# Performance work log

Hardware: AMD Instinct MI355X
Metric: run time of the kernel (lower is better)

The kernel has to match this reference:

```python
import jax, jax.numpy as jnp
import numpy as np

V = 6890   # SMPL vertices
J = 24     # SMPL joints
NB = 10    # betas
P = 207    # pose blendshape basis = (J-1)*9
B = 1024
PARENTS = np.array([-1, 0, 0, 0, 1, 2, 3, 4, 5, 6, 7, 8, 9, 9, 9, 12, 13, 14, 16, 17, 18, 19, 20, 21])


def setup_inputs() -> dict:
    key = jax.random.key(0)
    ks = jax.random.split(key, 9)
    pose_axis_angle = jax.random.normal(ks[0], (B, 69), dtype=jnp.float32) * 0.2
    betas = jax.random.normal(ks[1], (B, NB), dtype=jnp.float32)
    global_orient = jax.random.normal(ks[2], (B, 3), dtype=jnp.float32) * 0.2
    v_template = jax.random.normal(ks[3], (V, 3), dtype=jnp.float32)
    shapedirs = jax.random.normal(ks[4], (V, 3, NB), dtype=jnp.float32) * 0.01
    posedirs = jax.random.normal(ks[5], (P, V * 3), dtype=jnp.float32) * 0.01
    jr = jax.random.uniform(ks[6], (J, V), dtype=jnp.float32)
    J_regressor = jr / jr.sum(-1, keepdims=True)
    jr17 = jax.random.uniform(ks[7], (17, V), dtype=jnp.float32)
    J_regressor_h36m = jr17 / jr17.sum(-1, keepdims=True)
    w = jax.random.uniform(ks[8], (V, J), dtype=jnp.float32)
    lbs_weights = w / w.sum(-1, keepdims=True)
    return {
        'pose_axis_angle': pose_axis_angle, 'betas': betas, 'global_orient': global_orient,
        'v_template': v_template, 'shapedirs': shapedirs, 'posedirs': posedirs,
        'J_regressor': J_regressor, 'J_regressor_h36m': J_regressor_h36m,
        'lbs_weights': lbs_weights,
    }


def rodrigues(rvec):
    # rvec: [N,3] axis-angle -> [N,3,3] rotation matrices
    angle = jnp.linalg.norm(rvec + 1e-8, axis=-1, keepdims=True)  # [N,1]
    axis = rvec / angle
    s = jnp.sin(angle)[..., None]
    c = jnp.cos(angle)[..., None]
    rx, ry, rz = axis[..., 0], axis[..., 1], axis[..., 2]
    z = jnp.zeros_like(rx)
    K = jnp.stack([z, -rz, ry, rz, z, -rx, -ry, rx, z], axis=-1).reshape(-1, 3, 3)
    I = jnp.eye(3, dtype=rvec.dtype)
    return I + s * K + (1.0 - c) * (K @ K)


def _lbs(pose_axis_angle, betas, global_orient, v_template, shapedirs, posedirs,
         J_regressor, J_regressor_h36m, lbs_weights):
    b = betas.shape[0]
    full_pose = jnp.concatenate([global_orient, pose_axis_angle], axis=1)  # [B,72]
    # shape blendshapes
    v_shaped = v_template + jnp.einsum('bl,vkl->bvk', betas, shapedirs)    # [B,V,3]
    Jrest = jnp.einsum('jv,bvk->bjk', J_regressor, v_shaped)               # [B,J,3]
    # pose to rotation matrices
    rot_mats = rodrigues(full_pose.reshape(-1, 3)).reshape(b, J, 3, 3)
    I3 = jnp.eye(3, dtype=rot_mats.dtype)
    pose_feature = (rot_mats[:, 1:] - I3).reshape(b, P)                    # [B,207]
    v_posed = v_shaped + (pose_feature @ posedirs).reshape(b, V, 3)
    # kinematic tree FK
    rel = Jrest.at[:, 1:].add(-Jrest[:, PARENTS[1:]])                      # relative joint offsets
    T = (jnp.zeros((b, J, 4, 4), dtype=rot_mats.dtype)
         .at[..., :3, :3].set(rot_mats)
         .at[..., :3, 3].set(rel)
         .at[..., 3, 3].set(1.0))
    chain = [T[:, 0]]
    for i in range(1, J):
        chain.append(chain[int(PARENTS[i])] @ T[:, i])
    G = jnp.stack(chain, axis=1)                                           # [B,J,4,4]
    posed_joints = G[:, :, :3, 3]
    # remove rest-pose joint locations to get skinning transforms
    A = G.at[:, :, :3, 3].add(-jnp.einsum('bjmn,bjn->bjm', G[:, :, :3, :3], Jrest))
    # linear blend skinning
    Tv = jnp.einsum('vj,bjmn->bvmn', lbs_weights, A)                       # [B,V,4,4]
    verts = jnp.einsum('bvmn,bvn->bvm', Tv[:, :, :3, :3], v_posed) + Tv[:, :, :3, 3]
    joints_from_verts = jnp.einsum('jv,bvk->bjk', J_regressor_h36m, verts)
    return verts, posed_joints, rot_mats, joints_from_verts


def reference(pose_axis_angle, betas, global_orient, v_template, shapedirs, posedirs,
              J_regressor, J_regressor_h36m, lbs_weights):
    verts, joints, rot_mats, jfv = _lbs(pose_axis_angle, betas, global_orient, v_template,
                                        shapedirs, posedirs, J_regressor, J_regressor_h36m,
                                        lbs_weights)
    # transl is None -> root-center (root is detached in torch)
    root = jax.lax.stop_gradient(joints[:, :1])
    root17 = jax.lax.stop_gradient(jfv[:, :1])
    return verts - root, joints - root, rot_mats, jfv - root17
```

## Files before the change

kernel.cpp:

```cpp
#include <hip/hip_runtime.h>
#include <hip/hip_bf16.h>

constexpr int kB  = 1024;
constexpr int kV  = 6890;
constexpr int kJ  = 24;
constexpr int kNB = 10;
constexpr int kP  = 207;
constexpr int kH  = 17;

constexpr int kN   = kV * 3;
constexpr int kKP  = 224;
constexpr int kNT  = 1296;
constexpr int kNP  = kNT * 16;
constexpr int kVC  = 862;
constexpr int kTB  = 4;

constexpr int kJsBlocks = kJ * 8;
constexpr int kPbBlocks = kNP / 64;
constexpr int kVB = (kV + 255) / 256;
constexpr int kJB  = 4;

constexpr size_t O_VERTS  = 0;
constexpr size_t O_JOINTS = (size_t)kB * kV * 3;
constexpr size_t O_ROT    = O_JOINTS + (size_t)kB * kJ * 3;
constexpr size_t O_JFV    = O_ROT + (size_t)kB * kJ * 9;

constexpr size_t WS_JSP  = 0;
constexpr size_t WS_A    = 8192;
constexpr size_t WS_ROOT = WS_A + (size_t)kB * 288;
constexpr size_t WS_ASWZ = WS_ROOT + 4096;
constexpr size_t WS_BSWZ = WS_ASWZ + 114688;

typedef __attribute__((ext_vector_type(8))) short short8;
typedef __attribute__((ext_vector_type(4))) float float4v;

__device__ __forceinline__ unsigned short f2bf(float f) {
    unsigned u = __float_as_uint(f);
    unsigned r = (u + 0x7FFFu + ((u >> 16) & 1u)) >> 16;
    return (unsigned short)r;
}

__device__ __forceinline__ bool amb0_is_weights(const float* __restrict__ amb0) {
    float s = 0.f;
    #pragma unroll
    for (int i = 0; i < kJ; i++) s += amb0[i];
    return fabsf(s - 1.0f) < 0.5f;
}

__device__ __forceinline__ size_t a_idx(int mtile, int minr, int k) {
    int kt = k >> 5, quad = (k >> 3) & 3, kin = k & 7;
    return ((size_t)(mtile * 7 + kt)) * 512 + (size_t)(quad * 128 + minr * 8 + kin);
}

__global__ __launch_bounds__(256) void k_sfb(
    const float* __restrict__ amb0,
    const float* __restrict__ amb1,
    const float* __restrict__ sd,
    const float* __restrict__ vt,
    const float* __restrict__ pd,
    float* __restrict__ partial,
    unsigned short* __restrict__ bswz)
{
    __shared__ unsigned short lds[kKP][68];
    __shared__ float red[4][33];

    int t = threadIdx.x;

    if (blockIdx.x < kJsBlocks) {
        const float* Jreg = amb0_is_weights(amb0) ? amb1 : amb0;
        int j = blockIdx.x >> 3;
        int c = blockIdx.x & 7;
        int lane = t & 63;
        int wave = t >> 6;

        float acc[33];
        #pragma unroll
        for (int i = 0; i < 33; i++) acc[i] = 0.f;

        int vend = min(kVC * (c + 1), kV);
        for (int v = kVC * c + t; v < vend; v += 256) {
            float w = Jreg[j * kV + v];
            const float* sdp = sd + (size_t)v * 30;
            #pragma unroll
            for (int k = 0; k < 3; k++) {
                #pragma unroll
                for (int l = 0; l < kNB; l++)
                    acc[k * 11 + l] += w * sdp[k * 10 + l];
                acc[k * 11 + 10] += w * vt[v * 3 + k];
            }
        }
        #pragma unroll
        for (int off = 32; off > 0; off >>= 1) {
            #pragma unroll
            for (int i = 0; i < 33; i++)
                acc[i] += __shfl_down(acc[i], off, 64);
        }
        if (lane == 0) {
            #pragma unroll
            for (int i = 0; i < 33; i++) red[wave][i] = acc[i];
        }
        __syncthreads();
        if (t < 33) {
            float s = red[0][t] + red[1][t] + red[2][t] + red[3][t];
            partial[((size_t)j * 8 + c) * 33 + t] = s;
        }
    } else {
        int g = blockIdx.x - kJsBlocks;
        int n0 = g * 64;

        for (int kbase = 0; kbase < kKP; kbase += 4) {
            int k = kbase + (t >> 6);
            int nl = t & 63;
            int n = n0 + nl;
            float val = 0.f;
            if (n < kN) {
                if (k < kP)                 val = pd[(size_t)k * kN + n];
                else if (k < kP + kNB)      val = sd[(size_t)n * kNB + (k - kP)];
                else if (k == kP + kNB)     val = vt[n];
            }
            lds[k][nl] = f2bf(val);
        }
        __syncthreads();

        #pragma unroll 1
        for (int tt = 0; tt < 4; tt++) {
            int ntile = g * 4 + tt;
            #pragma unroll 1
            for (int kt = 0; kt < 7; kt++) {
                size_t base = ((size_t)ntile * 7 + kt) * 512;
                #pragma unroll
                for (int u = 0; u < 2; u++) {
                    int e = t * 2 + u;
                    int quad = e >> 7, rem = e & 127;
                    int nin = rem >> 3, kin = rem & 7;
                    int k = kt * 32 + quad * 8 + kin;
                    bswz[base + e] = lds[k][tt * 16 + nin];
                }
            }
        }
    }
}

__global__ __launch_bounds__(64) void k_pose(
    const float* __restrict__ pose,
    const float* __restrict__ betas,
    const float* __restrict__ gor,
    const float* __restrict__ jsp,
    float* __restrict__ wsA,
    float* __restrict__ wsRoot,
    unsigned short* __restrict__ aswz,
    float* __restrict__ out)
{
    __shared__ float Rsh[kJ][9];
    __shared__ float Jr[kJ][3];
    __shared__ float G[kJ][12];

    int b = blockIdx.x;
    int t = threadIdx.x;
    int mtile = b >> 4, minr = b & 15;

    if (t < kJ) {
        float rx, ry, rz;
        if (t == 0) {
            rx = gor[b * 3 + 0]; ry = gor[b * 3 + 1]; rz = gor[b * 3 + 2];
        } else {
            int o = b * 69 + (t - 1) * 3;
            rx = pose[o]; ry = pose[o + 1]; rz = pose[o + 2];
        }
        float ex = rx + 1e-8f, ey = ry + 1e-8f, ez = rz + 1e-8f;
        float ang = sqrtf(ex * ex + ey * ey + ez * ez);
        float x = rx / ang, y = ry / ang, z = rz / ang;
        float s = sinf(ang), c = cosf(ang), oc = 1.0f - c;
        float r[9];
        r[0] = 1.0f - oc * (y * y + z * z);
        r[1] = -s * z + oc * (x * y);
        r[2] =  s * y + oc * (x * z);
        r[3] =  s * z + oc * (x * y);
        r[4] = 1.0f - oc * (x * x + z * z);
        r[5] = -s * x + oc * (y * z);
        r[6] = -s * y + oc * (x * z);
        r[7] =  s * x + oc * (y * z);
        r[8] = 1.0f - oc * (x * x + y * y);
        #pragma unroll
        for (int i = 0; i < 9; i++) Rsh[t][i] = r[i];
        float* ro = out + O_ROT + (size_t)b * (kJ * 9) + (size_t)t * 9;
        #pragma unroll
        for (int i = 0; i < 9; i++) ro[i] = r[i];
        if (t >= 1) {
            #pragma unroll
            for (int i = 0; i < 9; i++) {
                int k = (t - 1) * 9 + i;
                float val = r[i] - ((i == 0 || i == 4 || i == 8) ? 1.0f : 0.0f);
                aswz[a_idx(mtile, minr, k)] = f2bf(val);
            }
        }
        float bt[kNB];
        #pragma unroll
        for (int l = 0; l < kNB; l++) bt[l] = betas[b * kNB + l];
        #pragma unroll
        for (int k2 = 0; k2 < 3; k2++) {
            float row[11];
            #pragma unroll
            for (int i = 0; i < 11; i++) row[i] = 0.f;
            #pragma unroll
            for (int c8 = 0; c8 < 8; c8++) {
                const float* pp = jsp + ((size_t)t * 8 + c8) * 33 + k2 * 11;
                #pragma unroll
                for (int i = 0; i < 11; i++) row[i] += pp[i];
            }
            float acc = row[10];
            #pragma unroll
            for (int l = 0; l < kNB; l++) acc += bt[l] * row[l];
            Jr[t][k2] = acc;
        }
    } else if (t < 41 + kJ) {
        int idx = t - kJ;
        if (idx < 17) {
            int k = kP + idx;
            float val = 0.f;
            if (idx < kNB)          val = betas[b * kNB + idx];
            else if (k == kP + kNB) val = 1.0f;
            aswz[a_idx(mtile, minr, k)] = f2bf(val);
        }
    }
    __syncthreads();

    if (t == 0) {
        const int par[kJ] = {-1,0,0,0,1,2,3,4,5,6,7,8,9,9,9,12,13,14,16,17,18,19,20,21};
        #pragma unroll
        for (int m = 0; m < 3; m++) {
            #pragma unroll
            for (int n = 0; n < 3; n++) G[0][m * 4 + n] = Rsh[0][m * 3 + n];
            G[0][m * 4 + 3] = Jr[0][m];
        }
        for (int i = 1; i < kJ; i++) {
            int p = par[i];
            float rel[3];
            #pragma unroll
            for (int k = 0; k < 3; k++) rel[k] = Jr[i][k] - Jr[p][k];
            #pragma unroll
            for (int m = 0; m < 3; m++) {
                float g0 = G[p][m * 4 + 0], g1 = G[p][m * 4 + 1], g2 = G[p][m * 4 + 2];
                #pragma unroll
                for (int n = 0; n < 3; n++) {
                    G[i][m * 4 + n] = g0 * Rsh[i][0 * 3 + n]
                                    + g1 * Rsh[i][1 * 3 + n]
                                    + g2 * Rsh[i][2 * 3 + n];
                }
                G[i][m * 4 + 3] = g0 * rel[0] + g1 * rel[1] + g2 * rel[2]
                                + G[p][m * 4 + 3];
            }
        }
    }
    __syncthreads();

    if (t < kJ) {
        float* Aj = wsA + (size_t)b * 288 + (size_t)t * 12;
        float* jo = out + O_JOINTS + (size_t)b * (kJ * 3) + (size_t)t * 3;
        #pragma unroll
        for (int m = 0; m < 3; m++) {
            float g0 = G[t][m * 4 + 0], g1 = G[t][m * 4 + 1], g2 = G[t][m * 4 + 2];
            Aj[m * 4 + 0] = g0;
            Aj[m * 4 + 1] = g1;
            Aj[m * 4 + 2] = g2;
            Aj[m * 4 + 3] = G[t][m * 4 + 3]
                          - (g0 * Jr[t][0] + g1 * Jr[t][1] + g2 * Jr[t][2]);
            jo[m] = G[t][m * 4 + 3] - G[0][m * 4 + 3];
        }
        if (t == 0) {
            #pragma unroll
            for (int k = 0; k < 3; k++) wsRoot[b * 3 + k] = G[0][k * 4 + 3];
        }
    }
}

__global__ __launch_bounds__(256) void k_gemm(
    const unsigned short* __restrict__ A,
    const unsigned short* __restrict__ B,
    float* __restrict__ out)
{
    int tid = threadIdx.x;
    int lane = tid & 63;
    int wid = tid >> 6;
    int m0t = blockIdx.y * 8 + (wid >> 1) * 4;
    int n0t = blockIdx.x * 8 + (wid & 1) * 4;

    float4v acc[4][4];
    #pragma unroll
    for (int i = 0; i < 4; i++)
        #pragma unroll
        for (int j = 0; j < 4; j++)
            acc[i][j] = (float4v){0.f, 0.f, 0.f, 0.f};

    #pragma unroll
    for (int kt = 0; kt < 7; kt++) {
        short8 a[4], b[4];
        #pragma unroll
        for (int i = 0; i < 4; i++)
            a[i] = *(const short8*)(A + ((size_t)(m0t + i) * 7 + kt) * 512 + lane * 8);
        #pragma unroll
        for (int j = 0; j < 4; j++)
            b[j] = *(const short8*)(B + ((size_t)(n0t + j) * 7 + kt) * 512 + lane * 8);
        #pragma unroll
        for (int i = 0; i < 4; i++)
            #pragma unroll
            for (int j = 0; j < 4; j++)
                acc[i][j] = __builtin_amdgcn_mfma_f32_16x16x32_bf16(
                    a[i], b[j], acc[i][j], 0, 0, 0);
    }

    int rbase = (lane >> 4) * 4;
    int col = lane & 15;
    #pragma unroll
    for (int i = 0; i < 4; i++) {
        #pragma unroll
        for (int j = 0; j < 4; j++) {
            int n = (n0t + j) * 16 + col;
            if (n < kN) {
                #pragma unroll
                for (int reg = 0; reg < 4; reg++) {
                    int brow = (m0t + i) * 16 + rbase + reg;
                    out[O_VERTS + (size_t)brow * kN + n] = acc[i][j][reg];
                }
            }
        }
    }
}

__global__ __launch_bounds__(256, 4) void k_lbs(
    const float* __restrict__ amb0,
    const float* __restrict__ amb1,
    const float* __restrict__ wsA,
    const float* __restrict__ wsRoot,
    float* __restrict__ out)
{
    const float* W = amb0_is_weights(amb0) ? amb0 : amb1;

    int t = threadIdx.x;
    int v = blockIdx.x * 256 + t;
    int b0 = blockIdx.y * kTB;
    bool active = (v < kV);
    int vc = active ? v : (kV - 1);

    float w[kJ];
    {
        const float4v* Wv4 = (const float4v*)(W + (size_t)vc * kJ);
        #pragma unroll
        for (int q = 0; q < 6; q++) {
            float4v x = Wv4[q];
            w[q * 4 + 0] = x[0]; w[q * 4 + 1] = x[1];
            w[q * 4 + 2] = x[2]; w[q * 4 + 3] = x[3];
        }
    }

    #pragma unroll 1
    for (int tb = 0; tb < kTB; tb++) {
        int b = b0 + tb;
        const float4v* A4 = (const float4v*)(wsA + (size_t)b * 288);
        float T0[4] = {0.f, 0.f, 0.f, 0.f};
        float T1[4] = {0.f, 0.f, 0.f, 0.f};
        float T2[4] = {0.f, 0.f, 0.f, 0.f};
        #pragma unroll
        for (int j = 0; j < kJ; j++) {
            float wj = w[j];
            float4v a0 = A4[j * 3 + 0];
            float4v a1 = A4[j * 3 + 1];
            float4v a2 = A4[j * 3 + 2];
            #pragma unroll
            for (int q = 0; q < 4; q++) {
                T0[q] += wj * a0[q];
                T1[q] += wj * a1[q];
                T2[q] += wj * a2[q];
            }
        }
        float r0 = wsRoot[(size_t)b * 3 + 0];
        float r1 = wsRoot[(size_t)b * 3 + 1];
        float r2 = wsRoot[(size_t)b * 3 + 2];
        if (active) {
            float* op = out + O_VERTS + ((size_t)b * kV + v) * 3;
            float x = op[0], y = op[1], z = op[2];
            op[0] = T0[0] * x + T0[1] * y + T0[2] * z + T0[3] - r0;
            op[1] = T1[0] * x + T1[1] * y + T1[2] * z + T1[3] - r1;
            op[2] = T2[0] * x + T2[1] * y + T2[2] * z + T2[3] - r2;
        }
    }
}

__global__ __launch_bounds__(1024) void k_jfv(
    const float* __restrict__ Jh,
    const float* __restrict__ verts,
    float* __restrict__ out)
{
    int b0 = blockIdx.x * kJB;
    int t = threadIdx.x;
    int wave = t >> 6, lane = t & 63;
    int j0 = wave;
    bool has2 = (wave == 0);

    float acc0[kJB][3], acc1[kJB][3];
    #pragma unroll
    for (int bb = 0; bb < kJB; bb++)
        #pragma unroll
        for (int k = 0; k < 3; k++) { acc0[bb][k] = 0.f; acc1[bb][k] = 0.f; }

    const float* Jr0 = Jh + (size_t)j0 * kV;
    const float* Jr1 = Jh + (size_t)16 * kV;

    for (int v = lane; v < kV; v += 64) {
        float w0 = Jr0[v];
        float w1 = has2 ? Jr1[v] : 0.f;
        #pragma unroll
        for (int bb = 0; bb < kJB; bb++) {
            const float* vp = verts + ((size_t)(b0 + bb) * kV + v) * 3;
            float vx = vp[0], vy = vp[1], vz = vp[2];
            acc0[bb][0] += w0 * vx; acc0[bb][1] += w0 * vy; acc0[bb][2] += w0 * vz;
            acc1[bb][0] += w1 * vx; acc1[bb][1] += w1 * vy; acc1[bb][2] += w1 * vz;
        }
    }
    #pragma unroll
    for (int off = 32; off > 0; off >>= 1) {
        #pragma unroll
        for (int bb = 0; bb < kJB; bb++)
            #pragma unroll
            for (int k = 0; k < 3; k++) {
                acc0[bb][k] += __shfl_down(acc0[bb][k], off, 64);
                acc1[bb][k] += __shfl_down(acc1[bb][k], off, 64);
            }
    }
    __shared__ float fin[kJB][52];
    if (lane == 0) {
        #pragma unroll
        for (int bb = 0; bb < kJB; bb++)
            #pragma unroll
            for (int k = 0; k < 3; k++) {
                fin[bb][j0 * 3 + k] = acc0[bb][k];
                if (has2) fin[bb][48 + k] = acc1[bb][k];
            }
    }
    __syncthreads();
    if (t < kJB * 51) {
        int bb = t / 51, i = t - bb * 51;
        out[O_JFV + (size_t)(b0 + bb) * 51 + i] = fin[bb][i] - fin[bb][i % 3];
    }
}

extern "C" void kernel_launch(void* const* d_in, const int* in_sizes, int n_in,
                              void* d_out, int out_size, void* d_ws, size_t ws_size,
                              hipStream_t stream) {
    const float *pose = nullptr, *betas = nullptr, *gor = nullptr, *vt = nullptr,
                *sd = nullptr, *pd = nullptr, *Jh = nullptr;
    const float *amb0 = nullptr, *amb1 = nullptr;
    for (int i = 0; i < n_in; i++) {
        const float* p = (const float*)d_in[i];
        switch (in_sizes[i]) {
            case 70656:   pose  = p; break;
            case 10240:   betas = p; break;
            case 3072:    gor   = p; break;
            case 20670:   vt    = p; break;
            case 206700:  sd    = p; break;
            case 4278690: pd    = p; break;
            case 117130:  Jh    = p; break;
            case 165360:  if (!amb0) amb0 = p; else amb1 = p; break;
            default: break;
        }
    }

    float* ws = (float*)d_ws;
    float* jsp     = ws + WS_JSP;
    float* wsA     = ws + WS_A;
    float* wsRoot  = ws + WS_ROOT;
    unsigned short* aswz = (unsigned short*)(ws + WS_ASWZ);
    unsigned short* bswz = (unsigned short*)(ws + WS_BSWZ);

    float* out = (float*)d_out;

    k_sfb  <<<dim3(kJsBlocks + kPbBlocks), dim3(256), 0, stream>>>(
        amb0, amb1, sd, vt, pd, jsp, bswz);
    k_pose <<<dim3(kB),                 dim3(64),  0, stream>>>(
        pose, betas, gor, jsp, wsA, wsRoot, aswz, out);
    k_gemm <<<dim3(kNT / 8, kB / 128),  dim3(256), 0, stream>>>(aswz, bswz, out);
    k_lbs  <<<dim3(kVB, kB / kTB),      dim3(256), 0, stream>>>(
        amb0, amb1, wsA, wsRoot, out);
    k_jfv  <<<dim3(kB / kJB),           dim3(1024), 0, stream>>>(
        Jh, out + O_VERTS, out);
}
```

Baseline: 312.6 us.

## Compute LBS blend transforms with split-bf16 MFMA instead of scalar FMA loops

k_pose now writes each batch's 24x12 skinning matrices as zero-padded hi/lo bf16 pairs. k_lbs then blends them with the per-vertex weights using three bf16 MFMAs (hi*hi, hi*lo, lo*hi) to get near-fp32 precision, stages the 12 transform values per vertex in LDS, and applies them. This replaces the per-thread 24x12 scalar FMA loop with matrix-core work and raises batches per block to 8. In exchange it adds LDS round-trips, two block barriers per batch and some precision loss from the split-bf16 scheme.

```diff
diff --git a/kernel.cpp b/kernel.cpp
--- a/kernel.cpp
+++ b/kernel.cpp
@@ -13,12 +13,11 @@
 constexpr int kNT  = 1296;
 constexpr int kNP  = kNT * 16;
 constexpr int kVC  = 862;
-constexpr int kTB  = 4;
 
 constexpr int kJsBlocks = kJ * 8;
 constexpr int kPbBlocks = kNP / 64;
-constexpr int kVB = (kV + 255) / 256;
 constexpr int kJB  = 4;
+constexpr int kLbsTB = 8;
 
 constexpr size_t O_VERTS  = 0;
 constexpr size_t O_JOINTS = (size_t)kB * kV * 3;
@@ -26,9 +25,10 @@
 constexpr size_t O_JFV    = O_ROT + (size_t)kB * kJ * 9;
 
 constexpr size_t WS_JSP  = 0;
-constexpr size_t WS_A    = 8192;
-constexpr size_t WS_ROOT = WS_A + (size_t)kB * 288;
-constexpr size_t WS_ASWZ = WS_ROOT + 4096;
+constexpr size_t WS_ROOT = 8192;
+constexpr size_t WS_ABHI = 16384;
+constexpr size_t WS_ABLO = WS_ABHI + 262144;
+constexpr size_t WS_ASWZ = WS_ABLO + 262144;
 constexpr size_t WS_BSWZ = WS_ASWZ + 114688;
 
 typedef __attribute__((ext_vector_type(8))) short short8;
@@ -38,6 +38,9 @@
     unsigned u = __float_as_uint(f);
     unsigned r = (u + 0x7FFFu + ((u >> 16) & 1u)) >> 16;
     return (unsigned short)r;
+}
+__device__ __forceinline__ float bf2f(unsigned short h) {
+    return __uint_as_float((unsigned)h << 16);
 }
 
 __device__ __forceinline__ bool amb0_is_weights(const float* __restrict__ amb0) {
@@ -146,14 +149,16 @@
     const float* __restrict__ betas,
     const float* __restrict__ gor,
     const float* __restrict__ jsp,
-    float* __restrict__ wsA,
     float* __restrict__ wsRoot,
     unsigned short* __restrict__ aswz,
+    unsigned short* __restrict__ abhi,
+    unsigned short* __restrict__ ablo,
     float* __restrict__ out)
 {
     __shared__ float Rsh[kJ][9];
     __shared__ float Jr[kJ][3];
     __shared__ float G[kJ][12];
+    __shared__ float Ash[kJ][12];
 
     int b = blockIdx.x;
     int t = threadIdx.x;
@@ -255,22 +260,38 @@
     __syncthreads();
 
     if (t < kJ) {
-        float* Aj = wsA + (size_t)b * 288 + (size_t)t * 12;
         float* jo = out + O_JOINTS + (size_t)b * (kJ * 3) + (size_t)t * 3;
         #pragma unroll
         for (int m = 0; m < 3; m++) {
             float g0 = G[t][m * 4 + 0], g1 = G[t][m * 4 + 1], g2 = G[t][m * 4 + 2];
-            Aj[m * 4 + 0] = g0;
-            Aj[m * 4 + 1] = g1;
-            Aj[m * 4 + 2] = g2;
-            Aj[m * 4 + 3] = G[t][m * 4 + 3]
-                          - (g0 * Jr[t][0] + g1 * Jr[t][1] + g2 * Jr[t][2]);
+            float tr = G[t][m * 4 + 3]
+                     - (g0 * Jr[t][0] + g1 * Jr[t][1] + g2 * Jr[t][2]);
+            Ash[t][m * 4 + 0] = g0;
+            Ash[t][m * 4 + 1] = g1;
+            Ash[t][m * 4 + 2] = g2;
+            Ash[t][m * 4 + 3] = tr;
             jo[m] = G[t][m * 4 + 3] - G[0][m * 4 + 3];
         }
         if (t == 0) {
             #pragma unroll
             for (int k = 0; k < 3; k++) wsRoot[b * 3 + k] = G[0][k * 4 + 3];
         }
+    }
+    __syncthreads();
+
+    {
+        short8 h8, l8;
+        #pragma unroll
+        for (int e = 0; e < 8; e++) {
+            int j = (t >> 4) * 8 + e;
+            int m = t & 15;
+            float val = (j < kJ && m < 12) ? Ash[j][m] : 0.f;
+            unsigned short h = f2bf(val);
+            h8[e] = (short)h;
+            l8[e] = (short)f2bf(val - bf2f(h));
+        }
+        *(short8*)(abhi + (size_t)b * 512 + t * 8) = h8;
+        *(short8*)(ablo + (size_t)b * 512 + t * 8) = l8;
     }
 }
 
@@ -327,62 +348,86 @@
     }
 }
 
-__global__ __launch_bounds__(256, 4) void k_lbs(
+__global__ __launch_bounds__(256) void k_lbs(
     const float* __restrict__ amb0,
     const float* __restrict__ amb1,
-    const float* __restrict__ wsA,
+    const unsigned short* __restrict__ abhi,
+    const unsigned short* __restrict__ ablo,
     const float* __restrict__ wsRoot,
     float* __restrict__ out)
 {
     const float* W = amb0_is_weights(amb0) ? amb0 : amb1;
+    __shared__ float ldsT[256 * 13];
 
     int t = threadIdx.x;
-    int v = blockIdx.x * 256 + t;
-    int b0 = blockIdx.y * kTB;
-    bool active = (v < kV);
-    int vc = active ? v : (kV - 1);
-
-    float w[kJ];
-    {
-        const float4v* Wv4 = (const float4v*)(W + (size_t)vc * kJ);
-        #pragma unroll
-        for (int q = 0; q < 6; q++) {
-            float4v x = Wv4[q];
-            w[q * 4 + 0] = x[0]; w[q * 4 + 1] = x[1];
-            w[q * 4 + 2] = x[2]; w[q * 4 + 3] = x[3];
-        }
-    }
+    int lane = t & 63, w = t >> 6;
+    int vb = blockIdx.x;
+    int b0 = blockIdx.y * kLbsTB;
+    int chunk = lane >> 4;
+
+    short8 wh[4], wl[4];
+    #pragma unroll
+    for (int i = 0; i < 4; i++) {
+        int row = vb * 256 + (w * 4 + i) * 16 + (lane & 15);
+        float vals[8];
+        if (chunk < 3 && row < kV) {
+            const float4v* p = (const float4v*)(W + (size_t)row * kJ + chunk * 8);
+            float4v x0 = p[0], x1 = p[1];
+            vals[0] = x0[0]; vals[1] = x0[1]; vals[2] = x0[2]; vals[3] = x0[3];
+            vals[4] = x1[0]; vals[5] = x1[1]; vals[6] = x1[2]; vals[7] = x1[3];
+        } else {
+            #pragma unroll
+            for (int e = 0; e < 8; e++) vals[e] = 0.f;
+        }
+        #pragma unroll
+        for (int e = 0; e < 8; e++) {
+            unsigned short h = f2bf(vals[e]);
+            wh[i][e] = (short)h;
+            wl[i][e] = (short)f2bf(vals[e] - bf2f(h));
+        }
+    }
+
+    int v = vb * 256 + t;
+    bool act = (v < kV);
+    int crow = (lane >> 4) * 4;
+    int ccol = lane & 15;
 
     #pragma unroll 1
-    for (int tb = 0; tb < kTB; tb++) {
+    for (int tb = 0; tb < kLbsTB; tb++) {
         int b = b0 + tb;
-        const float4v* A4 = (const float4v*)(wsA + (size_t)b * 288);
-        float T0[4] = {0.f, 0.f, 0.f, 0.f};
-        float T1[4] = {0.f, 0.f, 0.f, 0.f};
-        float T2[4] = {0.f, 0.f, 0.f, 0.f};
-        #pragma unroll
-        for (int j = 0; j < kJ; j++) {
-            float wj = w[j];
-            float4v a0 = A4[j * 3 + 0];
-            float4v a1 = A4[j * 3 + 1];
-            float4v a2 = A4[j * 3 + 2];
-            #pragma unroll
-            for (int q = 0; q < 4; q++) {
-                T0[q] += wj * a0[q];
-                T1[q] += wj * a1[q];
-                T2[q] += wj * a2[q];
-            }
-        }
-        float r0 = wsRoot[(size_t)b * 3 + 0];
-        float r1 = wsRoot[(size_t)b * 3 + 1];
-        float r2 = wsRoot[(size_t)b * 3 + 2];
-        if (active) {
-            float* op = out + O_VERTS + ((size_t)b * kV + v) * 3;
-            float x = op[0], y = op[1], z = op[2];
-            op[0] = T0[0] * x + T0[1] * y + T0[2] * z + T0[3] - r0;
-            op[1] = T1[0] * x + T1[1] * y + T1[2] * z + T1[3] - r1;
-            op[2] = T2[0] * x + T2[1] * y + T2[2] * z + T2[3] - r2;
-        }
+        short8 ah = *(const short8*)(abhi + (size_t)b * 512 + lane * 8);
+        short8 al = *(const short8*)(ablo + (size_t)b * 512 + lane * 8);
+
+        #pragma unroll
+        for (int i = 0; i < 4; i++) {
+            float4v acc = (float4v){0.f, 0.f, 0.f, 0.f};
+            acc = __builtin_amdgcn_mfma_f32_16x16x32_bf16(wl[i], ah, acc, 0, 0, 0);
+            acc = __builtin_amdgcn_mfma_f32_16x16x32_bf16(wh[i], al, acc, 0, 0, 0);
+            acc = __builtin_amdgcn_mfma_f32_16x16x32_bf16(wh[i], ah, acc, 0, 0, 0);
+            if (ccol < 12) {
+                int base = (w * 4 + i) * 16 * 13;
+                #pragma unroll
+                for (int reg = 0; reg < 4; reg++)
+                    ldsT[base + (crow + reg) * 13 + ccol] = acc[reg];
+            }
+        }
+        __syncthreads();
+
+        {
+            const float* T = &ldsT[t * 13];
+            float r0 = wsRoot[(size_t)b * 3 + 0];
+            float r1 = wsRoot[(size_t)b * 3 + 1];
+            float r2 = wsRoot[(size_t)b * 3 + 2];
+            if (act) {
+                float* op = out + O_VERTS + ((size_t)b * kV + v) * 3;
+                float x = op[0], y = op[1], z = op[2];
+                float o0 = T[0] * x + T[1] * y + T[2]  * z + T[3]  - r0;
+                float o1 = T[4] * x + T[5] * y + T[6]  * z + T[7]  - r1;
+                float o2 = T[8] * x + T[9] * y + T[10] * z + T[11] - r2;
+                op[0] = o0; op[1] = o1; op[2] = o2;
+            }
+        }
+        __syncthreads();
     }
 }
 
@@ -467,8 +512,9 @@
 
     float* ws = (float*)d_ws;
     float* jsp     = ws + WS_JSP;
-    float* wsA     = ws + WS_A;
     float* wsRoot  = ws + WS_ROOT;
+    unsigned short* abhi = (unsigned short*)(ws + WS_ABHI);
+    unsigned short* ablo = (unsigned short*)(ws + WS_ABLO);
     unsigned short* aswz = (unsigned short*)(ws + WS_ASWZ);
     unsigned short* bswz = (unsigned short*)(ws + WS_BSWZ);
 
@@ -477,10 +523,10 @@
     k_sfb  <<<dim3(kJsBlocks + kPbBlocks), dim3(256), 0, stream>>>(
         amb0, amb1, sd, vt, pd, jsp, bswz);
     k_pose <<<dim3(kB),                 dim3(64),  0, stream>>>(
-        pose, betas, gor, jsp, wsA, wsRoot, aswz, out);
+        pose, betas, gor, jsp, wsRoot, aswz, abhi, ablo, out);
     k_gemm <<<dim3(kNT / 8, kB / 128),  dim3(256), 0, stream>>>(aswz, bswz, out);
-    k_lbs  <<<dim3(kVB, kB / kTB),      dim3(256), 0, stream>>>(
-        amb0, amb1, wsA, wsRoot, out);
+    k_lbs  <<<dim3(27, kB / kLbsTB),    dim3(256), 0, stream>>>(
+        amb0, amb1, abhi, ablo, wsRoot, out);
     k_jfv  <<<dim3(kB / kJB),           dim3(1024), 0, stream>>>(
         Jh, out + O_VERTS, out);
 }
```

Result: faster. 283.7 us (-9.2%).
